# Kernel tuning notes

Measured on AMD Instinct MI355X. Metric: run time of the kernel, lower is better.

The kernel has to match this reference:

```python
import jax, jax.numpy as jnp
import numpy as np

D_MODEL = 256
N_LEVELS = 4
N_HEADS = 8
N_POINTS = 4
D_HEAD = D_MODEL // N_HEADS  # 32
BATCH = 8
SHAPES = np.array([[64, 64], [32, 32], [16, 16], [8, 8]], dtype=np.int32)
LEN_IN = int((SHAPES[:, 0] * SHAPES[:, 1]).sum())  # 5440
LEN_Q = LEN_IN
STARTS = np.concatenate([[0], np.cumsum(SHAPES[:, 0] * SHAPES[:, 1])[:-1]]).astype(np.int32)


def _offset_bias():
    # faithful _reset_parameters grid init for sampling_offsets bias
    thetas = np.arange(N_HEADS, dtype=np.float64) * (2.0 * np.pi / N_HEADS)
    grid = np.stack([np.cos(thetas), np.sin(thetas)], -1)
    grid = grid / np.abs(grid).max(-1, keepdims=True)
    grid = np.tile(grid[:, None, None, :], (1, N_LEVELS, N_POINTS, 1))
    grid = grid * (np.arange(N_POINTS) + 1)[None, None, :, None]
    return jnp.asarray(grid.reshape(-1), dtype=jnp.float32)


def setup_inputs() -> dict:
    key = jax.random.key(0)
    ks = jax.random.split(key, 8)
    s = 1.0 / np.sqrt(D_MODEL)
    return {
        "query": jax.random.normal(ks[0], (BATCH, LEN_Q, D_MODEL), jnp.float32),
        "reference_points": jax.random.uniform(ks[1], (BATCH, LEN_Q, N_LEVELS, 2), jnp.float32),
        "input_flatten": jax.random.normal(ks[2], (BATCH, LEN_IN, D_MODEL), jnp.float32),
        "input_spatial_shapes": jnp.asarray(SHAPES),
        "input_level_start_index": jnp.asarray(STARTS),
        "W_val": jax.random.normal(ks[3], (D_MODEL, D_MODEL), jnp.float32) * s,
        "b_val": jnp.zeros((D_MODEL,), jnp.float32),
        "W_off": jax.random.normal(ks[4], (D_MODEL, N_HEADS * N_LEVELS * N_POINTS * 2), jnp.float32) * 0.01,
        "b_off": _offset_bias(),
        "W_attn": jax.random.normal(ks[5], (D_MODEL, N_HEADS * N_LEVELS * N_POINTS), jnp.float32) * s,
        "b_attn": jnp.zeros((N_HEADS * N_LEVELS * N_POINTS,), jnp.float32),
        "W_out": jax.random.normal(ks[6], (D_MODEL, D_MODEL), jnp.float32) * s,
        "b_out": jnp.zeros((D_MODEL,), jnp.float32),
    }


def _ms_deform_attn_core(value, shapes_np, starts_np, sampling_locations, attention_weights):
    # value: (N, Lin, Hn, d); sampling_locations: (N, Lq, Hn, L, P, 2) in [0,1]
    # attention_weights: (N, Lq, Hn, L, P)
    n, lq = sampling_locations.shape[:2]
    value_t = jnp.transpose(value, (0, 2, 1, 3))  # (N, Hn, Lin, d)
    out = jnp.zeros((n, N_HEADS, lq, value.shape[-1]), value.dtype)
    for lvl in range(N_LEVELS):
        H, W = int(shapes_np[lvl, 0]), int(shapes_np[lvl, 1])
        st = int(starts_np[lvl])
        v = value_t[:, :, st:st + H * W]  # (N, Hn, H*W, d)
        loc = jnp.transpose(sampling_locations[:, :, :, lvl], (0, 2, 1, 3, 4))  # (N, Hn, Lq, P, 2)
        x = loc[..., 0] * W - 0.5
        y = loc[..., 1] * H - 0.5
        x0 = jnp.floor(x).astype(jnp.int32)
        y0 = jnp.floor(y).astype(jnp.int32)
        lx = x - x0
        ly = y - y0
        x1, y1 = x0 + 1, y0 + 1

        def gather(yc, xc):
            valid = (yc >= 0) & (yc < H) & (xc >= 0) & (xc < W)
            idx = jnp.clip(yc, 0, H - 1) * W + jnp.clip(xc, 0, W - 1)
            idx = idx.reshape(n, N_HEADS, -1)  # (N, Hn, Lq*P)
            g = jnp.take_along_axis(v, idx[..., None], axis=2)  # (N, Hn, Lq*P, d)
            return g * valid.reshape(n, N_HEADS, -1, 1)

        w00 = ((1 - lx) * (1 - ly)).reshape(n, N_HEADS, -1, 1)
        w01 = (lx * (1 - ly)).reshape(n, N_HEADS, -1, 1)
        w10 = ((1 - lx) * ly).reshape(n, N_HEADS, -1, 1)
        w11 = (lx * ly).reshape(n, N_HEADS, -1, 1)
        samp = (gather(y0, x0) * w00 + gather(y0, x1) * w01 +
                gather(y1, x0) * w10 + gather(y1, x1) * w11)
        samp = samp.reshape(n, N_HEADS, lq, N_POINTS, -1)
        aw = jnp.transpose(attention_weights[:, :, :, lvl], (0, 2, 1, 3))  # (N, Hn, Lq, P)
        out = out + (samp * aw[..., None]).sum(axis=3)
    return jnp.transpose(out, (0, 2, 1, 3)).reshape(n, lq, -1)


def reference(query, reference_points, input_flatten, input_spatial_shapes,
              input_level_start_index, W_val, b_val, W_off, b_off,
              W_attn, b_attn, W_out, b_out):
    shapes_np = np.asarray(input_spatial_shapes)
    starts_np = np.asarray(input_level_start_index)
    n, lq, _ = query.shape
    lin = input_flatten.shape[1]

    value = (input_flatten @ W_val + b_val).reshape(n, lin, N_HEADS, D_HEAD)
    off = (query @ W_off + b_off).reshape(n, lq, N_HEADS, N_LEVELS, N_POINTS, 2)
    attn = jax.nn.softmax((query @ W_attn + b_attn).reshape(n, lq, N_HEADS, N_LEVELS * N_POINTS), axis=-1)
    attn = attn.reshape(n, lq, N_HEADS, N_LEVELS, N_POINTS)

    # normalizer: (L, 2) as [W, H]
    normalizer = jnp.stack([input_spatial_shapes[:, 1], input_spatial_shapes[:, 0]], -1).astype(query.dtype)
    loc = reference_points[:, :, None, :, None, :] + off / normalizer[None, None, None, :, None, :]

    out = _ms_deform_attn_core(value, shapes_np, starts_np, loc, attn)
    return out @ W_out + b_out
```

## Files before the change

kernel.cpp:

```cpp
#include <hip/hip_runtime.h>

typedef unsigned short ushort;
typedef unsigned int uint;
typedef __bf16 bf16x8 __attribute__((ext_vector_type(8)));
typedef float floatx4 __attribute__((ext_vector_type(4)));
typedef float floatx2 __attribute__((ext_vector_type(2)));
typedef ushort ushort8 __attribute__((ext_vector_type(8)));
typedef uint uintx4 __attribute__((ext_vector_type(4)));

constexpr int LQ = 5440;
constexpr int ROWS = 43520;

__device__ __forceinline__ ushort f2b(float f) {
  union { float f; uint i; } v; v.f = f;
  uint r = v.i + 0x7FFFu + ((v.i >> 16) & 1u);
  return (ushort)(r >> 16);
}
__device__ __forceinline__ float blo(uint u) {
  union { uint i; float f; } v; v.i = u << 16; return v.f;
}
__device__ __forceinline__ float bhi(uint u) {
  union { uint i; float f; } v; v.i = u & 0xFFFF0000u; return v.f;
}
__device__ __forceinline__ void glds16(const ushort* g, ushort* l) {
  __builtin_amdgcn_global_load_lds(
      (const __attribute__((address_space(1))) void*)g,
      (__attribute__((address_space(3))) void*)l, 16, 0, 0);
}

__global__ __launch_bounds__(256) void wcast_kernel(
    const float* __restrict__ Wv, const float* __restrict__ Wo,
    const float* __restrict__ Wa, const float* __restrict__ Wu,
    ushort* __restrict__ Wt) {
  int k = threadIdx.x;
  int n = blockIdx.x;
  int m = blockIdx.y;
  const float* src = (m == 0) ? Wv : (m == 1) ? Wo : (m == 2) ? Wa : Wu;
  int N = (m == 2) ? 128 : 256;
  if (n >= N) return;
  size_t off = (size_t)m * 65536 - ((m == 3) ? 32768 : 0);
  Wt[off + (size_t)n * 256 + k] = f2b(src[(size_t)k * N + n]);
}

__global__ __launch_bounds__(256) void gemm_val64(
    const float* __restrict__ X, const ushort* __restrict__ WtV,
    const float* __restrict__ bval, ushort* __restrict__ value16) {
  __shared__ ushort At[2048];
  __shared__ ushort Bs[8192];
  const int t = threadIdx.x, lane = t & 63, wv = t >> 6;
  const int row_base = blockIdx.x * 64;
  floatx4 acc[4][4];
#pragma unroll
  for (int i = 0; i < 4; ++i)
#pragma unroll
    for (int j = 0; j < 4; ++j) acc[i][j] = floatx4{0.f, 0.f, 0.f, 0.f};

  const int r = t >> 2, q = t & 3;
  const float* ap = X + (size_t)(row_base + r) * 256 + q * 8;
  ushort* aslot = &At[((r >> 4) * 64 + q * 16 + (r & 15)) * 8];
  const ushort* bsrc[4];
#pragma unroll
  for (int i = 0; i < 4; ++i) {
    int l = t + 256 * i;
    int nt = l >> 6, qq = (l >> 4) & 3, n15 = l & 15;
    bsrc[i] = WtV + (size_t)(nt * 16 + n15) * 256 + qq * 8;
  }

  for (int k0 = 0; k0 < 256; k0 += 32) {
#pragma unroll
    for (int i = 0; i < 4; ++i) glds16(bsrc[i] + k0, &Bs[(t + 256 * i) * 8]);
    {
      float4 a0 = *(const float4*)(ap + k0), a1 = *(const float4*)(ap + k0 + 4);
      ushort8 u;
      u[0] = f2b(a0.x); u[1] = f2b(a0.y); u[2] = f2b(a0.z); u[3] = f2b(a0.w);
      u[4] = f2b(a1.x); u[5] = f2b(a1.y); u[6] = f2b(a1.z); u[7] = f2b(a1.w);
      *(ushort8*)aslot = u;
    }
    __syncthreads();
    bf16x8 af[4], bf[4];
#pragma unroll
    for (int ti = 0; ti < 4; ++ti)
      af[ti] = *(const bf16x8*)&At[(ti * 64 + lane) * 8];
#pragma unroll
    for (int tj = 0; tj < 4; ++tj)
      bf[tj] = *(const bf16x8*)&Bs[((4 * wv + tj) * 64 + lane) * 8];
#pragma unroll
    for (int ti = 0; ti < 4; ++ti)
#pragma unroll
      for (int tj = 0; tj < 4; ++tj)
        acc[ti][tj] = __builtin_amdgcn_mfma_f32_16x16x32_bf16(af[ti], bf[tj], acc[ti][tj], 0, 0, 0);
    __syncthreads();
  }
  const int quad = lane >> 4, l15 = lane & 15;
#pragma unroll
  for (int tj = 0; tj < 4; ++tj) {
    int gcol = (4 * wv + tj) * 16 + l15;
    float b = bval[gcol];
#pragma unroll
    for (int ti = 0; ti < 4; ++ti)
#pragma unroll
      for (int reg = 0; reg < 4; ++reg) {
        int grow = row_base + ti * 16 + quad * 4 + reg;
        value16[(size_t)grow * 256 + gcol] = f2b(acc[ti][tj][reg] + b);
      }
  }
}

__global__ __launch_bounds__(256) void gemm_oa_kernel(
    const float* __restrict__ Q, const ushort* __restrict__ WtOA,
    const float* __restrict__ boff, const float* __restrict__ battn,
    const float* __restrict__ refp, uint4* __restrict__ tblq) {
  __shared__ ushort At[2048];
  __shared__ ushort Bs[3072];
  const int t = threadIdx.x;
  const int lane = t & 63, wv = t >> 6;
  const int quad = lane >> 4, l15 = lane & 15;
  const int bx = blockIdx.x;
  const int row_base = (bx % 680) * 64;
  const int hp = bx / 680;
  floatx4 accO[4], accA[2];
#pragma unroll
  for (int p = 0; p < 4; ++p) accO[p] = floatx4{0.f, 0.f, 0.f, 0.f};
#pragma unroll
  for (int q = 0; q < 2; ++q) accA[q] = floatx4{0.f, 0.f, 0.f, 0.f};

  const int r = t >> 2, q = t & 3;
  const float* ap = Q + (size_t)(row_base + r) * 256 + q * 8;
  ushort* aslot = &At[((r >> 4) * 64 + q * 16 + (r & 15)) * 8];
  const ushort* osrc0;
  const ushort* osrc1 = nullptr;
  {
    int nt = t >> 6, qq = (t >> 4) & 3, n15 = t & 15;
    int nr = nt * 16 + n15;
    int grow_ = (nr < 64) ? (hp * 64 + nr) : (256 + hp * 32 + (nr - 64));
    osrc0 = WtOA + (size_t)grow_ * 256 + qq * 8;
  }
  if (t < 128) {
    int l = t + 256;
    int nt = l >> 6, qq = (l >> 4) & 3, n15 = l & 15;
    int nr = nt * 16 + n15;
    int grow_ = 256 + hp * 32 + (nr - 64);
    osrc1 = WtOA + (size_t)grow_ * 256 + qq * 8;
  }

  for (int k0 = 0; k0 < 256; k0 += 32) {
    glds16(osrc0 + k0, &Bs[t * 8]);
    if (t < 128) glds16(osrc1 + k0, &Bs[(t + 256) * 8]);
    {
      float4 a0 = *(const float4*)(ap + k0), a1 = *(const float4*)(ap + k0 + 4);
      ushort8 u;
      u[0] = f2b(a0.x); u[1] = f2b(a0.y); u[2] = f2b(a0.z); u[3] = f2b(a0.w);
      u[4] = f2b(a1.x); u[5] = f2b(a1.y); u[6] = f2b(a1.z); u[7] = f2b(a1.w);
      *(ushort8*)aslot = u;
    }
    __syncthreads();
    bf16x8 af = *(const bf16x8*)&At[(wv * 64 + lane) * 8];
#pragma unroll
    for (int p = 0; p < 4; ++p) {
      bf16x8 bf = *(const bf16x8*)&Bs[(p * 64 + lane) * 8];
      accO[p] = __builtin_amdgcn_mfma_f32_16x16x32_bf16(af, bf, accO[p], 0, 0, 0);
    }
#pragma unroll
    for (int qk = 0; qk < 2; ++qk) {
      bf16x8 bf = *(const bf16x8*)&Bs[((4 + qk) * 64 + lane) * 8];
      accA[qk] = __builtin_amdgcn_mfma_f32_16x16x32_bf16(af, bf, accA[qk], 0, 0, 0);
    }
    __syncthreads();
  }

  const int lp = l15, l = lp >> 2;
  const int wd = 64 >> l;
  const int st = (l == 0) ? 0 : (l == 1) ? 4096 : (l == 2) ? 5120 : 5376;
  const float lw = (float)wd;
  const int src = (quad << 4) | (2 * (lp & 7));
  float boO[4], boA[2];
#pragma unroll
  for (int p = 0; p < 4; ++p) boO[p] = boff[(4 * hp + p) * 16 + l15];
#pragma unroll
  for (int qk = 0; qk < 2; ++qk) boA[qk] = battn[(2 * hp + qk) * 16 + l15];

#pragma unroll
  for (int reg = 0; reg < 4; ++reg) {
    int grow = row_base + wv * 16 + quad * 4 + reg;
    float rx = refp[(size_t)grow * 8 + l * 2];
    float ry = refp[(size_t)grow * 8 + l * 2 + 1];
#pragma unroll
    for (int hh = 0; hh < 2; ++hh) {
      int h = 2 * hp + hh;
      float xa = accA[hh][reg] + boA[hh];
      float m = xa;
      m = fmaxf(m, __shfl_xor(m, 1, 64));
      m = fmaxf(m, __shfl_xor(m, 2, 64));
      m = fmaxf(m, __shfl_xor(m, 4, 64));
      m = fmaxf(m, __shfl_xor(m, 8, 64));
      float e = __expf(xa - m);
      float ssum = e;
      ssum += __shfl_xor(ssum, 1, 64);
      ssum += __shfl_xor(ssum, 2, 64);
      ssum += __shfl_xor(ssum, 4, 64);
      ssum += __shfl_xor(ssum, 8, 64);
      float aw = e / ssum;
      float v0 = accO[2 * hh][reg] + boO[2 * hh];
      float v1 = accO[2 * hh + 1][reg] + boO[2 * hh + 1];
      float x_lo = __shfl(v0, src, 64),     x_hi = __shfl(v1, src, 64);
      float y_lo = __shfl(v0, src | 1, 64), y_hi = __shfl(v1, src | 1, 64);
      float xo = (lp < 8) ? x_lo : x_hi;
      float yo = (lp < 8) ? y_lo : y_hi;
      float X = rx * lw + xo - 0.5f;
      float Y = ry * lw + yo - 0.5f;
      float fx = floorf(X), fy = floorf(Y);
      float lx = X - fx, ly = Y - fy;
      int x0 = (int)fx, y0 = (int)fy, x1 = x0 + 1, y1 = y0 + 1;
      int cx0 = min(max(x0, 0), wd - 1), cx1 = min(max(x1, 0), wd - 1);
      int cy0 = min(max(y0, 0), wd - 1), cy1 = min(max(y1, 0), wd - 1);
      float vx0 = (x0 >= 0 && x0 < wd) ? 1.f : 0.f;
      float vx1 = (x1 >= 0 && x1 < wd) ? 1.f : 0.f;
      float vy0 = (y0 >= 0 && y0 < wd) ? 1.f : 0.f;
      float vy1 = (y1 >= 0 && y1 < wd) ? 1.f : 0.f;
      float g00 = (1.f - lx) * (1.f - ly) * vx0 * vy0 * aw;
      float g01 = lx * (1.f - ly) * vx1 * vy0 * aw;
      float g10 = (1.f - lx) * ly * vx0 * vy1 * aw;
      float g11 = lx * ly * vx1 * vy1 * aw;
      uint i00 = st + cy0 * wd + cx0, i01 = st + cy0 * wd + cx1;
      uint i10 = st + cy1 * wd + cx0, i11 = st + cy1 * wd + cx1;
      uint4 ov;
      ov.x = i00 | (i01 << 16);
      ov.y = i10 | (i11 << 16);
      ov.z = (uint)f2b(g00) | ((uint)f2b(g01) << 16);
      ov.w = (uint)f2b(g10) | ((uint)f2b(g11) << 16);
      tblq[((size_t)grow * 8 + h) * 16 + lp] = ov;
    }
  }
}

__device__ __forceinline__ void accum4p(uint wz, uint ww, const uint2* __restrict__ vv,
                                        floatx2& x01, floatx2& x23) {
  const float ws[4] = {blo(wz), bhi(wz), blo(ww), bhi(ww)};
#pragma unroll
  for (int j = 0; j < 4; ++j) {
    floatx2 wj = {ws[j], ws[j]};
    floatx2 p = {blo(vv[j].x), bhi(vv[j].x)};
    floatx2 q = {blo(vv[j].y), bhi(vv[j].y)};
    x01 = __builtin_elementwise_fma(wj, p, x01);
    x23 = __builtin_elementwise_fma(wj, q, x23);
  }
}

__device__ __forceinline__ void consume_pair(
    const uintx4& S0, const uintx4& S1, const uintx4& S2, const uintx4& S3,
    const uint2* __restrict__ V, int brow0, int h, int s, int g,
    uint* __restrict__ coreo32) {
  floatx2 a01 = {0.f, 0.f}, a23 = {0.f, 0.f};
  floatx2 c01 = {0.f, 0.f}, c23 = {0.f, 0.f};
  accum4p(S0[2], S0[3], V + 0,  a01, a23);
  accum4p(S1[2], S1[3], V + 4,  a01, a23);
  accum4p(S2[2], S2[3], V + 8,  c01, c23);
  accum4p(S3[2], S3[3], V + 12, c01, c23);
#pragma unroll
  for (int m = 8; m <= 32; m <<= 1) {
    a01.x += __shfl_xor(a01.x, m, 64);
    a01.y += __shfl_xor(a01.y, m, 64);
    a23.x += __shfl_xor(a23.x, m, 64);
    a23.y += __shfl_xor(a23.y, m, 64);
    c01.x += __shfl_xor(c01.x, m, 64);
    c01.y += __shfl_xor(c01.y, m, 64);
    c23.x += __shfl_xor(c23.x, m, 64);
    c23.y += __shfl_xor(c23.y, m, 64);
  }
  if (s == 0) {
    uint2 o0, o1;
    o0.x = (uint)f2b(a01.x) | ((uint)f2b(a01.y) << 16);
    o0.y = (uint)f2b(a23.x) | ((uint)f2b(a23.y) << 16);
    o1.x = (uint)f2b(c01.x) | ((uint)f2b(c01.y) << 16);
    o1.y = (uint)f2b(c23.x) | ((uint)f2b(c23.y) << 16);
    *(uint2*)(coreo32 + (size_t)brow0 * 128 + h * 16 + g * 2) = o0;
    *(uint2*)(coreo32 + (size_t)(brow0 + 1) * 128 + h * 16 + g * 2) = o1;
  }
}

__global__ __launch_bounds__(512) void core_kernel(
    const ushort* __restrict__ value16, const uint4* __restrict__ tblq,
    uint* __restrict__ coreo32) {
  const int bx = blockIdx.x;
  const int b = bx & 7;
  const int tile = bx >> 3;
  const int t = threadIdx.x;
  const int h = t >> 6, lane = t & 63;
  const int s = lane >> 3, g = lane & 7;
  const uint g8 = (uint)(g << 3);
  const char* vbh = (const char*)value16 + (size_t)b * (LQ * 512) + (h << 6);
  const uintx4* tb = (const uintx4*)tblq;
  const int row0 = b * LQ + tile * 4;
  const size_t sb = ((size_t)row0 * 8 + h) * 16 + s;

  uintx4 A0 = __builtin_nontemporal_load(tb + sb);
  uintx4 A1 = __builtin_nontemporal_load(tb + sb + 8);
  uintx4 A2 = __builtin_nontemporal_load(tb + sb + 128);
  uintx4 A3 = __builtin_nontemporal_load(tb + sb + 136);
  uintx4 B0 = __builtin_nontemporal_load(tb + sb + 256);
  uintx4 B1 = __builtin_nontemporal_load(tb + sb + 264);
  uintx4 B2 = __builtin_nontemporal_load(tb + sb + 384);
  uintx4 B3 = __builtin_nontemporal_load(tb + sb + 392);

  uint2 VA[16], VB[16];
#define GL(d, idx16) d = *(const uint2*)(vbh + (((uint)(idx16) << 9) + g8))
  GL(VA[0],  (A0[0] & 0xFFFFu)); GL(VA[1],  (A0[0] >> 16));
  GL(VA[2],  (A0[1] & 0xFFFFu)); GL(VA[3],  (A0[1] >> 16));
  GL(VA[4],  (A1[0] & 0xFFFFu)); GL(VA[5],  (A1[0] >> 16));
  GL(VA[6],  (A1[1] & 0xFFFFu)); GL(VA[7],  (A1[1] >> 16));
  GL(VA[8],  (A2[0] & 0xFFFFu)); GL(VA[9],  (A2[0] >> 16));
  GL(VA[10], (A2[1] & 0xFFFFu)); GL(VA[11], (A2[1] >> 16));
  GL(VA[12], (A3[0] & 0xFFFFu)); GL(VA[13], (A3[0] >> 16));
  GL(VA[14], (A3[1] & 0xFFFFu)); GL(VA[15], (A3[1] >> 16));
  GL(VB[0],  (B0[0] & 0xFFFFu)); GL(VB[1],  (B0[0] >> 16));
  GL(VB[2],  (B0[1] & 0xFFFFu)); GL(VB[3],  (B0[1] >> 16));
  GL(VB[4],  (B1[0] & 0xFFFFu)); GL(VB[5],  (B1[0] >> 16));
  GL(VB[6],  (B1[1] & 0xFFFFu)); GL(VB[7],  (B1[1] >> 16));
  GL(VB[8],  (B2[0] & 0xFFFFu)); GL(VB[9],  (B2[0] >> 16));
  GL(VB[10], (B2[1] & 0xFFFFu)); GL(VB[11], (B2[1] >> 16));
  GL(VB[12], (B3[0] & 0xFFFFu)); GL(VB[13], (B3[0] >> 16));
  GL(VB[14], (B3[1] & 0xFFFFu)); GL(VB[15], (B3[1] >> 16));
#undef GL

  consume_pair(A0, A1, A2, A3, VA, row0,     h, s, g, coreo32);
  consume_pair(B0, B1, B2, B3, VB, row0 + 2, h, s, g, coreo32);
}

__global__ __launch_bounds__(256) void gemm_out64(
    const ushort* __restrict__ C, const ushort* __restrict__ WtU,
    const float* __restrict__ bout, float* __restrict__ out) {
  __shared__ ushort At[2048];
  __shared__ ushort Bs[8192];
  const int t = threadIdx.x, lane = t & 63, wv = t >> 6;
  const int row_base = blockIdx.x * 64;
  floatx4 acc[4][4];
#pragma unroll
  for (int i = 0; i < 4; ++i)
#pragma unroll
    for (int j = 0; j < 4; ++j) acc[i][j] = floatx4{0.f, 0.f, 0.f, 0.f};

  const ushort* asrc;
  {
    int mt = t >> 6, qq = (t >> 4) & 3, r15 = t & 15;
    asrc = C + (size_t)(row_base + mt * 16 + r15) * 256 + qq * 8;
  }
  const ushort* bsrc[4];
#pragma unroll
  for (int i = 0; i < 4; ++i) {
    int l = t + 256 * i;
    int nt = l >> 6, qq = (l >> 4) & 3, n15 = l & 15;
    bsrc[i] = WtU + (size_t)(nt * 16 + n15) * 256 + qq * 8;
  }

  for (int k0 = 0; k0 < 256; k0 += 32) {
    glds16(asrc + k0, &At[t * 8]);
#pragma unroll
    for (int i = 0; i < 4; ++i) glds16(bsrc[i] + k0, &Bs[(t + 256 * i) * 8]);
    __syncthreads();
    bf16x8 af[4], bf[4];
#pragma unroll
    for (int ti = 0; ti < 4; ++ti)
      af[ti] = *(const bf16x8*)&At[(ti * 64 + lane) * 8];
#pragma unroll
    for (int tj = 0; tj < 4; ++tj)
      bf[tj] = *(const bf16x8*)&Bs[((4 * wv + tj) * 64 + lane) * 8];
#pragma unroll
    for (int ti = 0; ti < 4; ++ti)
#pragma unroll
      for (int tj = 0; tj < 4; ++tj)
        acc[ti][tj] = __builtin_amdgcn_mfma_f32_16x16x32_bf16(af[ti], bf[tj], acc[ti][tj], 0, 0, 0);
    __syncthreads();
  }
  const int quad = lane >> 4, l15 = lane & 15;
#pragma unroll
  for (int tj = 0; tj < 4; ++tj) {
    int gcol = (4 * wv + tj) * 16 + l15;
    float b = bout[gcol];
#pragma unroll
    for (int ti = 0; ti < 4; ++ti)
#pragma unroll
      for (int reg = 0; reg < 4; ++reg) {
        int grow = row_base + ti * 16 + quad * 4 + reg;
        out[(size_t)grow * 256 + gcol] = acc[ti][tj][reg] + b;
      }
  }
}

extern "C" void kernel_launch(void* const* d_in, const int* in_sizes, int n_in,
                              void* d_out, int out_size, void* d_ws, size_t ws_size,
                              hipStream_t stream) {
  const float* query  = (const float*)d_in[0];
  const float* refp   = (const float*)d_in[1];
  const float* inpf   = (const float*)d_in[2];
  const float* W_val  = (const float*)d_in[5];
  const float* b_val  = (const float*)d_in[6];
  const float* W_off  = (const float*)d_in[7];
  const float* b_off  = (const float*)d_in[8];
  const float* W_attn = (const float*)d_in[9];
  const float* b_attn = (const float*)d_in[10];
  const float* W_out  = (const float*)d_in[11];
  const float* b_out  = (const float*)d_in[12];

  char* ws = (char*)d_ws;
  ushort* Wt    = (ushort*)ws;
  ushort* value = (ushort*)(ws + 1048576);
  uint4*  tbl   = (uint4*)(ws + 23330816);
  ushort* coreo = (ushort*)(ws + 112459776);

  dim3 blk(256);
  wcast_kernel<<<dim3(256, 4), blk, 0, stream>>>(W_val, W_off, W_attn, W_out, Wt);
  gemm_val64  <<<dim3(680), blk, 0, stream>>>(inpf, Wt, b_val, value);
  gemm_oa_kernel<<<dim3(2720), blk, 0, stream>>>(query, Wt + 65536, b_off, b_attn, refp, tbl);
  core_kernel <<<dim3(10880), dim3(512), 0, stream>>>(value, tbl, (uint*)coreo);
  gemm_out64  <<<dim3(680), blk, 0, stream>>>(coreo, Wt + 163840, b_out, (float*)d_out);
}
```

Baseline: 334.4 us.

## Fuse value/offset GEMMs into one launch and core sampling into output GEMM

```diff
diff --git a/kernel.cpp b/kernel.cpp
--- a/kernel.cpp
+++ b/kernel.cpp
@@ -42,13 +42,12 @@
   Wt[off + (size_t)n * 256 + k] = f2b(src[(size_t)k * N + n]);
 }
 
-__global__ __launch_bounds__(256) void gemm_val64(
-    const float* __restrict__ X, const ushort* __restrict__ WtV,
-    const float* __restrict__ bval, ushort* __restrict__ value16) {
-  __shared__ ushort At[2048];
-  __shared__ ushort Bs[8192];
+__device__ __forceinline__ void val_body(
+    int vbx, const float* __restrict__ X, const ushort* __restrict__ WtV,
+    const float* __restrict__ bval, ushort* __restrict__ value16,
+    ushort* At, ushort* Bs) {
   const int t = threadIdx.x, lane = t & 63, wv = t >> 6;
-  const int row_base = blockIdx.x * 64;
+  const int row_base = vbx * 64;
   floatx4 acc[4][4];
 #pragma unroll
   for (int i = 0; i < 4; ++i)
@@ -106,18 +105,16 @@
   }
 }
 
-__global__ __launch_bounds__(256) void gemm_oa_kernel(
-    const float* __restrict__ Q, const ushort* __restrict__ WtOA,
+__device__ __forceinline__ void oa_body(
+    int obx, const float* __restrict__ Q, const ushort* __restrict__ WtOA,
     const float* __restrict__ boff, const float* __restrict__ battn,
-    const float* __restrict__ refp, uint4* __restrict__ tblq) {
-  __shared__ ushort At[2048];
-  __shared__ ushort Bs[3072];
+    const float* __restrict__ refp, uint4* __restrict__ tblq,
+    ushort* At, ushort* Bs) {
   const int t = threadIdx.x;
   const int lane = t & 63, wv = t >> 6;
   const int quad = lane >> 4, l15 = lane & 15;
-  const int bx = blockIdx.x;
-  const int row_base = (bx % 680) * 64;
-  const int hp = bx / 680;
+  const int row_base = (obx % 680) * 64;
+  const int hp = obx / 680;
   floatx4 accO[4], accA[2];
 #pragma unroll
   for (int p = 0; p < 4; ++p) accO[p] = floatx4{0.f, 0.f, 0.f, 0.f};
@@ -233,6 +230,22 @@
   }
 }
 
+__global__ __launch_bounds__(256) void valoa_kernel(
+    const float* __restrict__ X, const float* __restrict__ Q,
+    const ushort* __restrict__ Wt,
+    const float* __restrict__ bval, const float* __restrict__ boff,
+    const float* __restrict__ battn, const float* __restrict__ refp,
+    ushort* __restrict__ value16, uint4* __restrict__ tblq) {
+  __shared__ ushort At[2048];
+  __shared__ ushort Bs[8192];
+  const int bx = blockIdx.x;
+  const int q5 = bx / 5, r5 = bx % 5;
+  if (r5 == 0)
+    val_body(q5, X, Wt, bval, value16, At, Bs);
+  else
+    oa_body(q5 * 4 + r5 - 1, Q, Wt + 65536, boff, battn, refp, tblq, At, Bs);
+}
+
 __device__ __forceinline__ void accum4p(uint wz, uint ww, const uint2* __restrict__ vv,
                                         floatx2& x01, floatx2& x23) {
   const float ws[4] = {blo(wz), bhi(wz), blo(ww), bhi(ww)};
@@ -246,10 +259,9 @@
   }
 }
 
-__device__ __forceinline__ void consume_pair(
+__device__ __forceinline__ void consume_pair_lds(
     const uintx4& S0, const uintx4& S1, const uintx4& S2, const uintx4& S3,
-    const uint2* __restrict__ V, int brow0, int h, int s, int g,
-    uint* __restrict__ coreo32) {
+    const uint2* __restrict__ V, int rl, int h, int s, int g, char* AtT) {
   floatx2 a01 = {0.f, 0.f}, a23 = {0.f, 0.f};
   floatx2 c01 = {0.f, 0.f}, c23 = {0.f, 0.f};
   accum4p(S0[2], S0[3], V + 0,  a01, a23);
@@ -273,115 +285,115 @@
     o0.y = (uint)f2b(a23.x) | ((uint)f2b(a23.y) << 16);
     o1.x = (uint)f2b(c01.x) | ((uint)f2b(c01.y) << 16);
     o1.y = (uint)f2b(c23.x) | ((uint)f2b(c23.y) << 16);
-    *(uint2*)(coreo32 + (size_t)brow0 * 128 + h * 16 + g * 2) = o0;
-    *(uint2*)(coreo32 + (size_t)(brow0 + 1) * 128 + h * 16 + g * 2) = o1;
-  }
-}
-
-__global__ __launch_bounds__(512) void core_kernel(
+    const int base = h * 64 + g * 8;
+    const int r1 = rl + 1;
+    *(uint2*)(AtT + ((rl * 512 + base) ^ ((rl & 7) << 4))) = o0;
+    *(uint2*)(AtT + ((r1 * 512 + base) ^ ((r1 & 7) << 4))) = o1;
+  }
+}
+
+__global__ __launch_bounds__(512) void core_out_kernel(
     const ushort* __restrict__ value16, const uint4* __restrict__ tblq,
-    uint* __restrict__ coreo32) {
+    const ushort* __restrict__ WtU, const float* __restrict__ bout,
+    float* __restrict__ out) {
+  __shared__ char AtT[32768];
+  __shared__ ushort Bs[8192];
   const int bx = blockIdx.x;
   const int b = bx & 7;
   const int tile = bx >> 3;
+  const int row_base = b * LQ + tile * 64;
   const int t = threadIdx.x;
   const int h = t >> 6, lane = t & 63;
   const int s = lane >> 3, g = lane & 7;
   const uint g8 = (uint)(g << 3);
   const char* vbh = (const char*)value16 + (size_t)b * (LQ * 512) + (h << 6);
   const uintx4* tb = (const uintx4*)tblq;
-  const int row0 = b * LQ + tile * 4;
-  const size_t sb = ((size_t)row0 * 8 + h) * 16 + s;
-
-  uintx4 A0 = __builtin_nontemporal_load(tb + sb);
-  uintx4 A1 = __builtin_nontemporal_load(tb + sb + 8);
-  uintx4 A2 = __builtin_nontemporal_load(tb + sb + 128);
-  uintx4 A3 = __builtin_nontemporal_load(tb + sb + 136);
-  uintx4 B0 = __builtin_nontemporal_load(tb + sb + 256);
-  uintx4 B1 = __builtin_nontemporal_load(tb + sb + 264);
-  uintx4 B2 = __builtin_nontemporal_load(tb + sb + 384);
-  uintx4 B3 = __builtin_nontemporal_load(tb + sb + 392);
-
-  uint2 VA[16], VB[16];
+
+  for (int it = 0; it < 16; ++it) {
+    const int row0 = row_base + it * 4;
+    const size_t sb = ((size_t)row0 * 8 + h) * 16 + s;
+
+    uintx4 A0 = __builtin_nontemporal_load(tb + sb);
+    uintx4 A1 = __builtin_nontemporal_load(tb + sb + 8);
+    uintx4 A2 = __builtin_nontemporal_load(tb + sb + 128);
+    uintx4 A3 = __builtin_nontemporal_load(tb + sb + 136);
+    uintx4 B0 = __builtin_nontemporal_load(tb + sb + 256);
+    uintx4 B1 = __builtin_nontemporal_load(tb + sb + 264);
+    uintx4 B2 = __builtin_nontemporal_load(tb + sb + 384);
+    uintx4 B3 = __builtin_nontemporal_load(tb + sb + 392);
+
+    uint2 VA[16], VB[16];
 #define GL(d, idx16) d = *(const uint2*)(vbh + (((uint)(idx16) << 9) + g8))
-  GL(VA[0],  (A0[0] & 0xFFFFu)); GL(VA[1],  (A0[0] >> 16));
-  GL(VA[2],  (A0[1] & 0xFFFFu)); GL(VA[3],  (A0[1] >> 16));
-  GL(VA[4],  (A1[0] & 0xFFFFu)); GL(VA[5],  (A1[0] >> 16));
-  GL(VA[6],  (A1[1] & 0xFFFFu)); GL(VA[7],  (A1[1] >> 16));
-  GL(VA[8],  (A2[0] & 0xFFFFu)); GL(VA[9],  (A2[0] >> 16));
-  GL(VA[10], (A2[1] & 0xFFFFu)); GL(VA[11], (A2[1] >> 16));
-  GL(VA[12], (A3[0] & 0xFFFFu)); GL(VA[13], (A3[0] >> 16));
-  GL(VA[14], (A3[1] & 0xFFFFu)); GL(VA[15], (A3[1] >> 16));
-  GL(VB[0],  (B0[0] & 0xFFFFu)); GL(VB[1],  (B0[0] >> 16));
-  GL(VB[2],  (B0[1] & 0xFFFFu)); GL(VB[3],  (B0[1] >> 16));
-  GL(VB[4],  (B1[0] & 0xFFFFu)); GL(VB[5],  (B1[0] >> 16));
-  GL(VB[6],  (B1[1] & 0xFFFFu)); GL(VB[7],  (B1[1] >> 16));
-  GL(VB[8],  (B2[0] & 0xFFFFu)); GL(VB[9],  (B2[0] >> 16));
-  GL(VB[10], (B2[1] & 0xFFFFu)); GL(VB[11], (B2[1] >> 16));
-  GL(VB[12], (B3[0] & 0xFFFFu)); GL(VB[13], (B3[0] >> 16));
-  GL(VB[14], (B3[1] & 0xFFFFu)); GL(VB[15], (B3[1] >> 16));
+    GL(VA[0],  (A0[0] & 0xFFFFu)); GL(VA[1],  (A0[0] >> 16));
+    GL(VA[2],  (A0[1] & 0xFFFFu)); GL(VA[3],  (A0[1] >> 16));
+    GL(VA[4],  (A1[0] & 0xFFFFu)); GL(VA[5],  (A1[0] >> 16));
+    GL(VA[6],  (A1[1] & 0xFFFFu)); GL(VA[7],  (A1[1] >> 16));
+    GL(VA[8],  (A2[0] & 0xFFFFu)); GL(VA[9],  (A2[0] >> 16));
+    GL(VA[10], (A2[1] & 0xFFFFu)); GL(VA[11], (A2[1] >> 16));
+    GL(VA[12], (A3[0] & 0xFFFFu)); GL(VA[13], (A3[0] >> 16));
+    GL(VA[14], (A3[1] & 0xFFFFu)); GL(VA[15], (A3[1] >> 16));
+    GL(VB[0],  (B0[0] & 0xFFFFu)); GL(VB[1],  (B0[0] >> 16));
+    GL(VB[2],  (B0[1] & 0xFFFFu)); GL(VB[3],  (B0[1] >> 16));
+    GL(VB[4],  (B1[0] & 0xFFFFu)); GL(VB[5],  (B1[0] >> 16));
+    GL(VB[6],  (B1[1] & 0xFFFFu)); GL(VB[7],  (B1[1] >> 16));
+    GL(VB[8],  (B2[0] & 0xFFFFu)); GL(VB[9],  (B2[0] >> 16));
+    GL(VB[10], (B2[1] & 0xFFFFu)); GL(VB[11], (B2[1] >> 16));
+    GL(VB[12], (B3[0] & 0xFFFFu)); GL(VB[13], (B3[0] >> 16));
+    GL(VB[14], (B3[1] & 0xFFFFu)); GL(VB[15], (B3[1] >> 16));
 #undef GL
 
-  consume_pair(A0, A1, A2, A3, VA, row0,     h, s, g, coreo32);
-  consume_pair(B0, B1, B2, B3, VB, row0 + 2, h, s, g, coreo32);
-}
-
-__global__ __launch_bounds__(256) void gemm_out64(
-    const ushort* __restrict__ C, const ushort* __restrict__ WtU,
-    const float* __restrict__ bout, float* __restrict__ out) {
-  __shared__ ushort At[2048];
-  __shared__ ushort Bs[8192];
-  const int t = threadIdx.x, lane = t & 63, wv = t >> 6;
-  const int row_base = blockIdx.x * 64;
-  floatx4 acc[4][4];
+    consume_pair_lds(A0, A1, A2, A3, VA, it * 4,     h, s, g, AtT);
+    consume_pair_lds(B0, B1, B2, B3, VB, it * 4 + 2, h, s, g, AtT);
+  }
+  __syncthreads();
+
+  const int wv = h;
+  floatx4 acc[4][2];
 #pragma unroll
   for (int i = 0; i < 4; ++i)
 #pragma unroll
-    for (int j = 0; j < 4; ++j) acc[i][j] = floatx4{0.f, 0.f, 0.f, 0.f};
-
-  const ushort* asrc;
-  {
-    int mt = t >> 6, qq = (t >> 4) & 3, r15 = t & 15;
-    asrc = C + (size_t)(row_base + mt * 16 + r15) * 256 + qq * 8;
-  }
-  const ushort* bsrc[4];
-#pragma unroll
-  for (int i = 0; i < 4; ++i) {
-    int l = t + 256 * i;
+    for (int j = 0; j < 2; ++j) acc[i][j] = floatx4{0.f, 0.f, 0.f, 0.f};
+
+  const ushort* bsrc[2];
+#pragma unroll
+  for (int i = 0; i < 2; ++i) {
+    int l = t + 512 * i;
     int nt = l >> 6, qq = (l >> 4) & 3, n15 = l & 15;
     bsrc[i] = WtU + (size_t)(nt * 16 + n15) * 256 + qq * 8;
   }
 
   for (int k0 = 0; k0 < 256; k0 += 32) {
-    glds16(asrc + k0, &At[t * 8]);
-#pragma unroll
-    for (int i = 0; i < 4; ++i) glds16(bsrc[i] + k0, &Bs[(t + 256 * i) * 8]);
-    __syncthreads();
-    bf16x8 af[4], bf[4];
+#pragma unroll
+    for (int i = 0; i < 2; ++i) glds16(bsrc[i] + k0, &Bs[(t + 512 * i) * 8]);
+    __syncthreads();
+    bf16x8 af[4], bf[2];
+#pragma unroll
+    for (int ti = 0; ti < 4; ++ti) {
+      int row = ti * 16 + (lane & 15);
+      int lin = row * 512 + k0 * 2 + (lane >> 4) * 16;
+      af[ti] = *(const bf16x8*)(AtT + (lin ^ ((row & 7) << 4)));
+    }
+#pragma unroll
+    for (int tj = 0; tj < 2; ++tj)
+      bf[tj] = *(const bf16x8*)&Bs[((2 * wv + tj) * 64 + lane) * 8];
 #pragma unroll
     for (int ti = 0; ti < 4; ++ti)
-      af[ti] = *(const bf16x8*)&At[(ti * 64 + lane) * 8];
-#pragma unroll
-    for (int tj = 0; tj < 4; ++tj)
-      bf[tj] = *(const bf16x8*)&Bs[((4 * wv + tj) * 64 + lane) * 8];
-#pragma unroll
-    for (int ti = 0; ti < 4; ++ti)
-#pragma unroll
-      for (int tj = 0; tj < 4; ++tj)
+#pragma unroll
+      for (int tj = 0; tj < 2; ++tj)
         acc[ti][tj] = __builtin_amdgcn_mfma_f32_16x16x32_bf16(af[ti], bf[tj], acc[ti][tj], 0, 0, 0);
     __syncthreads();
   }
   const int quad = lane >> 4, l15 = lane & 15;
 #pragma unroll
-  for (int tj = 0; tj < 4; ++tj) {
-    int gcol = (4 * wv + tj) * 16 + l15;
-    float b = bout[gcol];
+  for (int tj = 0; tj < 2; ++tj) {
+    int gcol = (2 * wv + tj) * 16 + l15;
+    float bb = bout[gcol];
 #pragma unroll
     for (int ti = 0; ti < 4; ++ti)
 #pragma unroll
       for (int reg = 0; reg < 4; ++reg) {
         int grow = row_base + ti * 16 + quad * 4 + reg;
-        out[(size_t)grow * 256 + gcol] = acc[ti][tj][reg] + b;
+        out[(size_t)grow * 256 + gcol] = acc[ti][tj][reg] + bb;
       }
   }
 }
@@ -405,12 +417,11 @@
   ushort* Wt    = (ushort*)ws;
   ushort* value = (ushort*)(ws + 1048576);
   uint4*  tbl   = (uint4*)(ws + 23330816);
-  ushort* coreo = (ushort*)(ws + 112459776);
 
   dim3 blk(256);
   wcast_kernel<<<dim3(256, 4), blk, 0, stream>>>(W_val, W_off, W_attn, W_out, Wt);
-  gemm_val64  <<<dim3(680), blk, 0, stream>>>(inpf, Wt, b_val, value);
-  gemm_oa_kernel<<<dim3(2720), blk, 0, stream>>>(query, Wt + 65536, b_off, b_attn, refp, tbl);
-  core_kernel <<<dim3(10880), dim3(512), 0, stream>>>(value, tbl, (uint*)coreo);
-  gemm_out64  <<<dim3(680), blk, 0, stream>>>(coreo, Wt + 163840, b_out, (float*)d_out);
-}
+  valoa_kernel<<<dim3(3400), blk, 0, stream>>>(inpf, query, Wt, b_val, b_off,
+                                               b_attn, refp, value, tbl);
+  core_out_kernel<<<dim3(680), dim3(512), 0, stream>>>(value, tbl, Wt + 163840,
+                                                       b_out, (float*)d_out);
+}
```

After: 347.1 us. 1.04x slower.

## Merge value and offset/attention GEMMs into one launch; simplify core sampling kernel

Applied to the files above, without the earlier changes.

```diff
diff --git a/kernel.cpp b/kernel.cpp
--- a/kernel.cpp
+++ b/kernel.cpp
@@ -42,13 +42,12 @@
   Wt[off + (size_t)n * 256 + k] = f2b(src[(size_t)k * N + n]);
 }
 
-__global__ __launch_bounds__(256) void gemm_val64(
-    const float* __restrict__ X, const ushort* __restrict__ WtV,
-    const float* __restrict__ bval, ushort* __restrict__ value16) {
-  __shared__ ushort At[2048];
-  __shared__ ushort Bs[8192];
+__device__ __forceinline__ void val_body(
+    int vbx, const float* __restrict__ X, const ushort* __restrict__ WtV,
+    const float* __restrict__ bval, ushort* __restrict__ value16,
+    ushort* At, ushort* Bs) {
   const int t = threadIdx.x, lane = t & 63, wv = t >> 6;
-  const int row_base = blockIdx.x * 64;
+  const int row_base = vbx * 64;
   floatx4 acc[4][4];
 #pragma unroll
   for (int i = 0; i < 4; ++i)
@@ -106,18 +105,16 @@
   }
 }
 
-__global__ __launch_bounds__(256) void gemm_oa_kernel(
-    const float* __restrict__ Q, const ushort* __restrict__ WtOA,
+__device__ __forceinline__ void oa_body(
+    int obx, const float* __restrict__ Q, const ushort* __restrict__ WtOA,
     const float* __restrict__ boff, const float* __restrict__ battn,
-    const float* __restrict__ refp, uint4* __restrict__ tblq) {
-  __shared__ ushort At[2048];
-  __shared__ ushort Bs[3072];
+    const float* __restrict__ refp, uint4* __restrict__ tblq,
+    ushort* At, ushort* Bs) {
   const int t = threadIdx.x;
   const int lane = t & 63, wv = t >> 6;
   const int quad = lane >> 4, l15 = lane & 15;
-  const int bx = blockIdx.x;
-  const int row_base = (bx % 680) * 64;
-  const int hp = bx / 680;
+  const int row_base = (obx % 680) * 64;
+  const int hp = obx / 680;
   floatx4 accO[4], accA[2];
 #pragma unroll
   for (int p = 0; p < 4; ++p) accO[p] = floatx4{0.f, 0.f, 0.f, 0.f};
@@ -233,49 +230,20 @@
   }
 }
 
-__device__ __forceinline__ void accum4p(uint wz, uint ww, const uint2* __restrict__ vv,
-                                        floatx2& x01, floatx2& x23) {
-  const float ws[4] = {blo(wz), bhi(wz), blo(ww), bhi(ww)};
-#pragma unroll
-  for (int j = 0; j < 4; ++j) {
-    floatx2 wj = {ws[j], ws[j]};
-    floatx2 p = {blo(vv[j].x), bhi(vv[j].x)};
-    floatx2 q = {blo(vv[j].y), bhi(vv[j].y)};
-    x01 = __builtin_elementwise_fma(wj, p, x01);
-    x23 = __builtin_elementwise_fma(wj, q, x23);
-  }
-}
-
-__device__ __forceinline__ void consume_pair(
-    const uintx4& S0, const uintx4& S1, const uintx4& S2, const uintx4& S3,
-    const uint2* __restrict__ V, int brow0, int h, int s, int g,
-    uint* __restrict__ coreo32) {
-  floatx2 a01 = {0.f, 0.f}, a23 = {0.f, 0.f};
-  floatx2 c01 = {0.f, 0.f}, c23 = {0.f, 0.f};
-  accum4p(S0[2], S0[3], V + 0,  a01, a23);
-  accum4p(S1[2], S1[3], V + 4,  a01, a23);
-  accum4p(S2[2], S2[3], V + 8,  c01, c23);
-  accum4p(S3[2], S3[3], V + 12, c01, c23);
-#pragma unroll
-  for (int m = 8; m <= 32; m <<= 1) {
-    a01.x += __shfl_xor(a01.x, m, 64);
-    a01.y += __shfl_xor(a01.y, m, 64);
-    a23.x += __shfl_xor(a23.x, m, 64);
-    a23.y += __shfl_xor(a23.y, m, 64);
-    c01.x += __shfl_xor(c01.x, m, 64);
-    c01.y += __shfl_xor(c01.y, m, 64);
-    c23.x += __shfl_xor(c23.x, m, 64);
-    c23.y += __shfl_xor(c23.y, m, 64);
-  }
-  if (s == 0) {
-    uint2 o0, o1;
-    o0.x = (uint)f2b(a01.x) | ((uint)f2b(a01.y) << 16);
-    o0.y = (uint)f2b(a23.x) | ((uint)f2b(a23.y) << 16);
-    o1.x = (uint)f2b(c01.x) | ((uint)f2b(c01.y) << 16);
-    o1.y = (uint)f2b(c23.x) | ((uint)f2b(c23.y) << 16);
-    *(uint2*)(coreo32 + (size_t)brow0 * 128 + h * 16 + g * 2) = o0;
-    *(uint2*)(coreo32 + (size_t)(brow0 + 1) * 128 + h * 16 + g * 2) = o1;
-  }
+__global__ __launch_bounds__(256) void valoa_kernel(
+    const float* __restrict__ X, const float* __restrict__ Q,
+    const ushort* __restrict__ Wt,
+    const float* __restrict__ bval, const float* __restrict__ boff,
+    const float* __restrict__ battn, const float* __restrict__ refp,
+    ushort* __restrict__ value16, uint4* __restrict__ tblq) {
+  __shared__ ushort At[2048];
+  __shared__ ushort Bs[8192];
+  const int bx = blockIdx.x;
+  const int q5 = bx / 5, r5 = bx % 5;
+  if (r5 == 0)
+    val_body(q5, X, Wt, bval, value16, At, Bs);
+  else
+    oa_body(q5 * 4 + r5 - 1, Q, Wt + 65536, boff, battn, refp, tblq, At, Bs);
 }
 
 __global__ __launch_bounds__(512) void core_kernel(
@@ -283,47 +251,55 @@
     uint* __restrict__ coreo32) {
   const int bx = blockIdx.x;
   const int b = bx & 7;
-  const int tile = bx >> 3;
+  const int pr = bx >> 3;
+  const int brow0 = b * LQ + pr * 2;
   const int t = threadIdx.x;
   const int h = t >> 6, lane = t & 63;
   const int s = lane >> 3, g = lane & 7;
-  const uint g8 = (uint)(g << 3);
-  const char* vbh = (const char*)value16 + (size_t)b * (LQ * 512) + (h << 6);
-  const uintx4* tb = (const uintx4*)tblq;
-  const int row0 = b * LQ + tile * 4;
-  const size_t sb = ((size_t)row0 * 8 + h) * 16 + s;
-
-  uintx4 A0 = __builtin_nontemporal_load(tb + sb);
-  uintx4 A1 = __builtin_nontemporal_load(tb + sb + 8);
-  uintx4 A2 = __builtin_nontemporal_load(tb + sb + 128);
-  uintx4 A3 = __builtin_nontemporal_load(tb + sb + 136);
-  uintx4 B0 = __builtin_nontemporal_load(tb + sb + 256);
-  uintx4 B1 = __builtin_nontemporal_load(tb + sb + 264);
-  uintx4 B2 = __builtin_nontemporal_load(tb + sb + 384);
-  uintx4 B3 = __builtin_nontemporal_load(tb + sb + 392);
-
-  uint2 VA[16], VB[16];
-#define GL(d, idx16) d = *(const uint2*)(vbh + (((uint)(idx16) << 9) + g8))
-  GL(VA[0],  (A0[0] & 0xFFFFu)); GL(VA[1],  (A0[0] >> 16));
-  GL(VA[2],  (A0[1] & 0xFFFFu)); GL(VA[3],  (A0[1] >> 16));
-  GL(VA[4],  (A1[0] & 0xFFFFu)); GL(VA[5],  (A1[0] >> 16));
-  GL(VA[6],  (A1[1] & 0xFFFFu)); GL(VA[7],  (A1[1] >> 16));
-  GL(VA[8],  (A2[0] & 0xFFFFu)); GL(VA[9],  (A2[0] >> 16));
-  GL(VA[10], (A2[1] & 0xFFFFu)); GL(VA[11], (A2[1] >> 16));
-  GL(VA[12], (A3[0] & 0xFFFFu)); GL(VA[13], (A3[0] >> 16));
-  GL(VA[14], (A3[1] & 0xFFFFu)); GL(VA[15], (A3[1] >> 16));
-  GL(VB[0],  (B0[0] & 0xFFFFu)); GL(VB[1],  (B0[0] >> 16));
-  GL(VB[2],  (B0[1] & 0xFFFFu)); GL(VB[3],  (B0[1] >> 16));
-  GL(VB[4],  (B1[0] & 0xFFFFu)); GL(VB[5],  (B1[0] >> 16));
-  GL(VB[6],  (B1[1] & 0xFFFFu)); GL(VB[7],  (B1[1] >> 16));
-  GL(VB[8],  (B2[0] & 0xFFFFu)); GL(VB[9],  (B2[0] >> 16));
-  GL(VB[10], (B2[1] & 0xFFFFu)); GL(VB[11], (B2[1] >> 16));
-  GL(VB[12], (B3[0] & 0xFFFFu)); GL(VB[13], (B3[0] >> 16));
-  GL(VB[14], (B3[1] & 0xFFFFu)); GL(VB[15], (B3[1] >> 16));
-#undef GL
-
-  consume_pair(A0, A1, A2, A3, VA, row0,     h, s, g, coreo32);
-  consume_pair(B0, B1, B2, B3, VB, row0 + 2, h, s, g, coreo32);
+  const size_t sb = ((size_t)brow0 * 8 + h) * 16;
+  uint4 sA0 = tblq[sb + s];
+  uint4 sA1 = tblq[sb + 8 + s];
+  uint4 sB0 = tblq[sb + 128 + s];
+  uint4 sB1 = tblq[sb + 136 + s];
+  const uint2* vb = (const uint2*)value16 + (size_t)b * (LQ * 64) + h * 8 + g;
+  float a[4] = {0.f, 0.f, 0.f, 0.f};
+  float c[4] = {0.f, 0.f, 0.f, 0.f};
+
+  auto proc = [&](const uint4& sl, float* ac) {
+    uint2 v00 = vb[(size_t)(sl.x & 0xFFFFu) * 64];
+    uint2 v01 = vb[(size_t)(sl.x >> 16) * 64];
+    uint2 v10 = vb[(size_t)(sl.y & 0xFFFFu) * 64];
+    uint2 v11 = vb[(size_t)(sl.y >> 16) * 64];
+    float w00 = blo(sl.z), w01 = bhi(sl.z), w10 = blo(sl.w), w11 = bhi(sl.w);
+    ac[0] = fmaf(w00, blo(v00.x), ac[0]); ac[1] = fmaf(w00, bhi(v00.x), ac[1]);
+    ac[2] = fmaf(w00, blo(v00.y), ac[2]); ac[3] = fmaf(w00, bhi(v00.y), ac[3]);
+    ac[0] = fmaf(w01, blo(v01.x), ac[0]); ac[1] = fmaf(w01, bhi(v01.x), ac[1]);
+    ac[2] = fmaf(w01, blo(v01.y), ac[2]); ac[3] = fmaf(w01, bhi(v01.y), ac[3]);
+    ac[0] = fmaf(w10, blo(v10.x), ac[0]); ac[1] = fmaf(w10, bhi(v10.x), ac[1]);
+    ac[2] = fmaf(w10, blo(v10.y), ac[2]); ac[3] = fmaf(w10, bhi(v10.y), ac[3]);
+    ac[0] = fmaf(w11, blo(v11.x), ac[0]); ac[1] = fmaf(w11, bhi(v11.x), ac[1]);
+    ac[2] = fmaf(w11, blo(v11.y), ac[2]); ac[3] = fmaf(w11, bhi(v11.y), ac[3]);
+  };
+  proc(sA0, a); proc(sA1, a);
+  proc(sB0, c); proc(sB1, c);
+
+#pragma unroll
+  for (int m = 8; m <= 32; m <<= 1) {
+#pragma unroll
+    for (int i = 0; i < 4; ++i) {
+      a[i] += __shfl_xor(a[i], m, 64);
+      c[i] += __shfl_xor(c[i], m, 64);
+    }
+  }
+  if (s == 0) {
+    uint2 o0, o1;
+    o0.x = (uint)f2b(a[0]) | ((uint)f2b(a[1]) << 16);
+    o0.y = (uint)f2b(a[2]) | ((uint)f2b(a[3]) << 16);
+    o1.x = (uint)f2b(c[0]) | ((uint)f2b(c[1]) << 16);
+    o1.y = (uint)f2b(c[2]) | ((uint)f2b(c[3]) << 16);
+    *(uint2*)(coreo32 + (size_t)brow0 * 128 + h * 16 + g * 2) = o0;
+    *(uint2*)(coreo32 + (size_t)(brow0 + 1) * 128 + h * 16 + g * 2) = o1;
+  }
 }
 
 __global__ __launch_bounds__(256) void gemm_out64(
@@ -409,8 +385,8 @@
 
   dim3 blk(256);
   wcast_kernel<<<dim3(256, 4), blk, 0, stream>>>(W_val, W_off, W_attn, W_out, Wt);
-  gemm_val64  <<<dim3(680), blk, 0, stream>>>(inpf, Wt, b_val, value);
-  gemm_oa_kernel<<<dim3(2720), blk, 0, stream>>>(query, Wt + 65536, b_off, b_attn, refp, tbl);
-  core_kernel <<<dim3(10880), dim3(512), 0, stream>>>(value, tbl, (uint*)coreo);
+  valoa_kernel<<<dim3(3400), blk, 0, stream>>>(inpf, query, Wt, b_val, b_off,
+                                               b_attn, refp, value, tbl);
+  core_kernel <<<dim3(21760), dim3(512), 0, stream>>>(value, tbl, (uint*)coreo);
   gemm_out64  <<<dim3(680), blk, 0, stream>>>(coreo, Wt + 163840, b_out, (float*)d_out);
 }
```

Result: slower. 346.0 us (+3.5%).
